# Optimization experiments

Measured on AMD Instinct MI355X. Metric: run time of the kernel, lower is better.

The kernel has to match this reference:

```python
import jax, jax.numpy as jnp
import numpy as np

B, H, LK, D = 8, 16, 4096, 128


def setup_inputs() -> dict:
    key = jax.random.key(0)
    ks = jax.random.split(key, 9)
    s = 1.0 / np.sqrt(D)
    return {
        "Q": jax.random.normal(ks[0], (B, H, 1, D), dtype=jnp.float32),
        "K": jax.random.normal(ks[1], (B, H, LK, D), dtype=jnp.float32),
        "V": jax.random.normal(ks[2], (B, H, LK, D), dtype=jnp.float32),
        "mask": jax.random.randint(ks[3], (B, H, 1, LK), 0, 2, dtype=jnp.int32),
        "scale": 1,  # accepted but unused by the original forward
        "W_pre": jax.random.normal(ks[4], (D, D), dtype=jnp.float32) * s,
        "b_pre": jax.random.normal(ks[5], (D,), dtype=jnp.float32) * s,
        "W_q": jax.random.normal(ks[6], (D, D), dtype=jnp.float32) * s,
        "W_v": jax.random.normal(ks[7], (D, 1), dtype=jnp.float32) * s,
    }


def reference(Q, K, V, mask, scale, W_pre, b_pre, W_q, W_v):
    # precompute = linear_pre(K): [B,H,LK,D]
    pre = jnp.einsum("bhkd,de->bhke", K, W_pre) + b_pre
    # targetT = linear_q(Q): [B,H,1,D], broadcast-added over keys
    tq = jnp.einsum("bhqd,de->bhqe", Q, W_q)
    tmp = jnp.tanh(pre + tq)  # [B,H,LK,D]
    # energy = linear_v(tmp) reshaped to [B,H,1,LK]
    energy = jnp.einsum("bhkd,d->bhk", tmp, W_v[:, 0])[:, :, None, :]
    m = mask.astype(energy.dtype)
    energy = energy * (1.0 - m) + m * (-1e6)
    score = jax.nn.softmax(energy, axis=-1)  # [B,H,1,LK]
    context = jnp.matmul(score, V)  # [B,H,1,D]
    return (context, score, pre)
```

## Files before the change

kernel.cpp:

```cpp
#include <hip/hip_runtime.h>
#include <hip/hip_bf16.h>
#include <math.h>

#define B_   8
#define H_   16
#define BH_  (B_*H_)
#define LK_  4096
#define D_   128

#define SEG   16
#define KSEG  (LK_/SEG)

typedef __attribute__((ext_vector_type(8))) short bf16x8;
typedef __attribute__((ext_vector_type(4))) float f32x4;

__device__ __forceinline__ float fast_tanh(float x) {
    float ax = fabsf(x);
    float e  = __expf(2.0f * ax);
    float r  = 1.0f - __fdividef(2.0f, e + 1.0f);
    return copysignf(r, x);
}

__device__ __forceinline__ void cvt_hilo(float x, unsigned short& h, unsigned short& l) {
    __hip_bfloat16 bh = __float2bfloat16(x);
    unsigned short hu = __builtin_bit_cast(unsigned short, bh);
    float hf = __uint_as_float((unsigned int)hu << 16);
    __hip_bfloat16 bl = __float2bfloat16(x - hf);
    h = hu;
    l = __builtin_bit_cast(unsigned short, bl);
}

__device__ __forceinline__ void cvt8(const float4 a, const float4 b, bf16x8& h, bf16x8& l) {
    float xs[8] = {a.x, a.y, a.z, a.w, b.x, b.y, b.z, b.w};
#pragma unroll
    for (int j = 0; j < 8; ++j) {
        unsigned short hu, lu;
        cvt_hilo(xs[j], hu, lu);
        h[j] = (short)hu;
        l[j] = (short)lu;
    }
}

__global__ void pack_kernel(const float* __restrict__ Wpre,
                            unsigned short* __restrict__ Bhi,
                            unsigned short* __restrict__ Blo) {
    int idx  = blockIdx.x * 256 + threadIdx.x;
    int j    = idx & 7;
    int lane = (idx >> 3) & 63;
    int nt   = (idx >> 9) & 7;
    int ks   = idx >> 12;
    int k    = ks * 32 + (lane >> 4) * 8 + j;
    int n    = nt * 16 + (lane & 15);
    unsigned short h, l;
    cvt_hilo(Wpre[k * D_ + n], h, l);
    Bhi[idx] = h;
    Blo[idx] = l;
}

__global__ void tq_kernel(const float* __restrict__ Q,
                          const float* __restrict__ Wq,
                          float* __restrict__ tq) {
    int bh = blockIdx.x;
    int e  = threadIdx.x;
    const float* q = Q + bh * D_;
    float acc = 0.0f;
#pragma unroll 8
    for (int d = 0; d < D_; ++d)
        acc = fmaf(q[d], Wq[d * D_ + e], acc);
    tq[bh * D_ + e] = acc;
}

__global__ void __launch_bounds__(256, 2)
main_kernel(const float* __restrict__ K,
            const unsigned short* __restrict__ Whi,
            const unsigned short* __restrict__ Wlo,
            const float* __restrict__ bpre,
            const float* __restrict__ Wv,
            const float* __restrict__ tqg,
            float* __restrict__ pre_out,
            float* __restrict__ energy_out) {
    const int t    = threadIdx.x;
    const int lane = t & 63;
    const int wv_  = t >> 6;
    const int kg   = wv_ & 1;
    const int eh   = wv_ >> 1;
    const int l15  = lane & 15;
    const int lg   = lane >> 4;
    const int bh   = blockIdx.y;
    const int kblk = blockIdx.x * 256;

    __shared__ float eLDS[2][2][64];

    bf16x8 wfh[4][4], wfl[4][4];
#pragma unroll
    for (int ks = 0; ks < 4; ++ks)
#pragma unroll
        for (int et = 0; et < 4; ++et) {
            size_t idx = (((size_t)ks * 8 + eh * 4 + et) * 64 + lane) * 8;
            wfh[ks][et] = *(const bf16x8*)(Whi + idx);
            wfl[ks][et] = *(const bf16x8*)(Wlo + idx);
        }

    float4 bpv[4], tqv[4], wvv[4];
#pragma unroll
    for (int et = 0; et < 4; ++et) {
        const int e0 = eh * 64 + et * 16 + lg * 4;
        bpv[et] = *(const float4*)(bpre + e0);
        tqv[et] = *(const float4*)(tqg + bh * D_ + e0);
        wvv[et] = *(const float4*)(Wv + e0);
    }

    const float* Kw = K + ((size_t)bh * LK_ + kblk + kg * 32 + l15) * D_ + lg * 8;

    float4 rw[2][2][2];
#pragma unroll
    for (int kt = 0; kt < 2; ++kt) {
        rw[0][kt][0] = *(const float4*)(Kw + (size_t)kt * 16 * D_);
        rw[0][kt][1] = *(const float4*)(Kw + (size_t)kt * 16 * D_ + 4);
    }

#pragma unroll
    for (int it = 0; it < 4; ++it) {
        f32x4 acc[2][4];
#pragma unroll
        for (int kt = 0; kt < 2; ++kt)
#pragma unroll
            for (int et = 0; et < 4; ++et)
                acc[kt][et] = (f32x4){0.f, 0.f, 0.f, 0.f};

#pragma unroll
        for (int ks = 0; ks < 4; ++ks) {
            const int cur = ks & 1, nxt = cur ^ 1;
            if (ks < 3) {
#pragma unroll
                for (int kt = 0; kt < 2; ++kt) {
                    const float* p = Kw + ((size_t)it * 64 + kt * 16) * D_ + (ks + 1) * 32;
                    rw[nxt][kt][0] = *(const float4*)p;
                    rw[nxt][kt][1] = *(const float4*)(p + 4);
                }
            } else if (it < 3) {
#pragma unroll
                for (int kt = 0; kt < 2; ++kt) {
                    const float* p = Kw + ((size_t)(it + 1) * 64 + kt * 16) * D_;
                    rw[nxt][kt][0] = *(const float4*)p;
                    rw[nxt][kt][1] = *(const float4*)(p + 4);
                }
            }
            bf16x8 kh[2], kl[2];
            cvt8(rw[cur][0][0], rw[cur][0][1], kh[0], kl[0]);
            cvt8(rw[cur][1][0], rw[cur][1][1], kh[1], kl[1]);
#pragma unroll
            for (int kt = 0; kt < 2; ++kt)
#pragma unroll
                for (int et = 0; et < 4; ++et) {
                    acc[kt][et] = __builtin_amdgcn_mfma_f32_16x16x32_bf16(wfh[ks][et], kh[kt], acc[kt][et], 0, 0, 0);
                    acc[kt][et] = __builtin_amdgcn_mfma_f32_16x16x32_bf16(wfl[ks][et], kh[kt], acc[kt][et], 0, 0, 0);
                    acc[kt][et] = __builtin_amdgcn_mfma_f32_16x16x32_bf16(wfh[ks][et], kl[kt], acc[kt][et], 0, 0, 0);
                }
        }

        const int kb = kblk + it * 64 + kg * 32;
#pragma unroll
        for (int kt = 0; kt < 2; ++kt) {
            float* pb = pre_out + ((size_t)bh * LK_ + kb + kt * 16 + l15) * D_ + eh * 64 + lg * 4;
            float ep = 0.0f;
#pragma unroll
            for (int et = 0; et < 4; ++et) {
                f32x4 a = acc[kt][et];
                f32x4 v;
                v[0] = a[0] + bpv[et].x;
                v[1] = a[1] + bpv[et].y;
                v[2] = a[2] + bpv[et].z;
                v[3] = a[3] + bpv[et].w;
                __builtin_nontemporal_store(v, (f32x4*)(pb + et * 16));
                ep = fmaf(fast_tanh(v[0] + tqv[et].x), wvv[et].x, ep);
                ep = fmaf(fast_tanh(v[1] + tqv[et].y), wvv[et].y, ep);
                ep = fmaf(fast_tanh(v[2] + tqv[et].z), wvv[et].z, ep);
                ep = fmaf(fast_tanh(v[3] + tqv[et].w), wvv[et].w, ep);
            }
            ep += __shfl_xor(ep, 16, 64);
            ep += __shfl_xor(ep, 32, 64);
            if (lg == 0)
                eLDS[it & 1][eh][kg * 32 + kt * 16 + l15] = ep;
        }
        asm volatile("s_waitcnt lgkmcnt(0)\n\ts_barrier" ::: "memory");
        if (t < 64) {
            float e = eLDS[it & 1][0][t] + eLDS[it & 1][1][t];
            energy_out[(size_t)bh * LK_ + kblk + it * 64 + t] = e;
        }
    }
}

__global__ void ml_kernel(const float* __restrict__ energy,
                          const int* __restrict__ mask,
                          float* __restrict__ ml) {
    const int bh = blockIdx.x;
    const int t  = threadIdx.x;
    const float* e = energy + (size_t)bh * LK_;
    const int*   m = mask   + (size_t)bh * LK_;

    float mx = -1e30f;
    for (int k = t; k < LK_; k += 256) {
        float v = m[k] ? -1.0e6f : e[k];
        mx = fmaxf(mx, v);
    }
#pragma unroll
    for (int off = 32; off > 0; off >>= 1)
        mx = fmaxf(mx, __shfl_xor(mx, off, 64));
    __shared__ float wmax[4];
    if ((t & 63) == 0) wmax[t >> 6] = mx;
    __syncthreads();
    mx = fmaxf(fmaxf(wmax[0], wmax[1]), fmaxf(wmax[2], wmax[3]));

    float sum = 0.0f;
    for (int k = t; k < LK_; k += 256) {
        float v = m[k] ? -1.0e6f : e[k];
        sum += __expf(v - mx);
    }
#pragma unroll
    for (int off = 32; off > 0; off >>= 1)
        sum += __shfl_xor(sum, off, 64);
    __shared__ float wsum[4];
    if ((t & 63) == 0) wsum[t >> 6] = sum;
    __syncthreads();
    if (t == 0) {
        ml[bh * 2]     = mx;
        ml[bh * 2 + 1] = wsum[0] + wsum[1] + wsum[2] + wsum[3];
    }
}

__global__ void score_ctx_kernel(const float* __restrict__ energy,
                                 const int* __restrict__ mask,
                                 const float* __restrict__ V,
                                 const float* __restrict__ ml,
                                 float* __restrict__ score_out,
                                 float* __restrict__ part) {
    const int seg = blockIdx.x;
    const int bh  = blockIdx.y;
    const int t   = threadIdx.x;
    const int k0  = seg * KSEG;

    __shared__ float sc[KSEG];
    __shared__ float pl[8][136];

    const float mx  = ml[bh * 2];
    const float inv = 1.0f / ml[bh * 2 + 1];

    {
        const size_t gi = (size_t)bh * LK_ + k0 + t;
        float v = mask[gi] ? -1.0e6f : energy[gi];
        float s = __expf(v - mx) * inv;
        sc[t] = s;
        score_out[gi] = s;
    }
    __syncthreads();

    const int d4 = t & 31;
    const int g  = t >> 5;
    const float* Vb = V + ((size_t)bh * LK_ + k0) * D_ + d4 * 4;
    float4 a = make_float4(0.f, 0.f, 0.f, 0.f);
#pragma unroll 4
    for (int kk = g; kk < KSEG; kk += 8) {
        float4 vv = *(const float4*)(Vb + (size_t)kk * D_);
        float s = sc[kk];
        a.x = fmaf(s, vv.x, a.x);
        a.y = fmaf(s, vv.y, a.y);
        a.z = fmaf(s, vv.z, a.z);
        a.w = fmaf(s, vv.w, a.w);
    }
    *(float4*)&pl[g][d4 * 4] = a;
    __syncthreads();

    if (t < 128) {
        float s = 0.0f;
#pragma unroll
        for (int gg = 0; gg < 8; ++gg)
            s += pl[gg][t];
        part[((size_t)bh * SEG + seg) * D_ + t] = s;
    }
}

__global__ void combine_kernel(const float* __restrict__ part,
                               float* __restrict__ ctx) {
    const int bh = blockIdx.x;
    const int d  = threadIdx.x;
    float s = 0.0f;
#pragma unroll
    for (int g = 0; g < SEG; ++g)
        s += part[((size_t)bh * SEG + g) * D_ + d];
    ctx[bh * D_ + d] = s;
}

extern "C" void kernel_launch(void* const* d_in, const int* in_sizes, int n_in,
                              void* d_out, int out_size, void* d_ws, size_t ws_size,
                              hipStream_t stream) {
    const float* Q    = (const float*)d_in[0];
    const float* K    = (const float*)d_in[1];
    const float* V    = (const float*)d_in[2];
    const int*   mask = (const int*)  d_in[3];
    const float* Wpre = (const float*)d_in[5];
    const float* bpre = (const float*)d_in[6];
    const float* Wq   = (const float*)d_in[7];
    const float* Wv   = (const float*)d_in[8];

    float* out   = (float*)d_out;
    float* ctx   = out;
    float* score = out + (size_t)BH_ * D_;
    float* pre   = score + (size_t)BH_ * LK_;

    float* w    = (float*)d_ws;
    float* tq   = w;
    float* ml   = tq + (size_t)BH_ * D_;
    float* part = ml + 2 * BH_;
    unsigned short* Whi = (unsigned short*)(part + (size_t)BH_ * SEG * D_);
    unsigned short* Wlo = Whi + 16384;

    hipLaunchKernelGGL(pack_kernel, dim3(64), dim3(256), 0, stream, Wpre, Whi, Wlo);
    hipLaunchKernelGGL(tq_kernel, dim3(BH_), dim3(D_), 0, stream, Q, Wq, tq);
    hipLaunchKernelGGL(main_kernel, dim3(LK_ / 256, BH_), dim3(256), 0, stream,
                       K, Whi, Wlo, bpre, Wv, tq, pre, score);
    hipLaunchKernelGGL(ml_kernel, dim3(BH_), dim3(256), 0, stream, score, mask, ml);
    hipLaunchKernelGGL(score_ctx_kernel, dim3(SEG, BH_), dim3(256), 0, stream,
                       score, mask, V, ml, score, part);
    hipLaunchKernelGGL(combine_kernel, dim3(BH_), dim3(D_), 0, stream, part, ctx);
}
```

Baseline: 242.1 us.

## Drop per-iteration barrier, use packed bf16 conversion and three-deep K prefetch

The main kernel no longer combines the two half-energy partials through shared memory behind a barrier on every iteration. Each wave half now writes its partial to a separate global buffer, and the following kernels add the two halves when they read them. The hi/lo bf16 split of K now uses the packed v_cvt_pk_bf16_f32 instruction instead of scalar conversions. The K register prefetch grows from double to triple buffering. In exchange the downstream kernels do extra global reads, and the main kernel holds more registers, which may strain occupancy at launch bounds 256,2.

```diff
diff --git a/kernel.cpp b/kernel.cpp
--- a/kernel.cpp
+++ b/kernel.cpp
@@ -13,12 +13,19 @@
 
 typedef __attribute__((ext_vector_type(8))) short bf16x8;
 typedef __attribute__((ext_vector_type(4))) float f32x4;
+typedef __attribute__((ext_vector_type(4))) unsigned int u32x4;
 
 __device__ __forceinline__ float fast_tanh(float x) {
     float ax = fabsf(x);
     float e  = __expf(2.0f * ax);
     float r  = 1.0f - __fdividef(2.0f, e + 1.0f);
     return copysignf(r, x);
+}
+
+__device__ __forceinline__ unsigned int cvtpk(float lo, float hi) {
+    unsigned int r;
+    asm("v_cvt_pk_bf16_f32 %0, %1, %2" : "=v"(r) : "v"(lo), "v"(hi));
+    return r;
 }
 
 __device__ __forceinline__ void cvt_hilo(float x, unsigned short& h, unsigned short& l) {
@@ -31,14 +38,22 @@
 }
 
 __device__ __forceinline__ void cvt8(const float4 a, const float4 b, bf16x8& h, bf16x8& l) {
-    float xs[8] = {a.x, a.y, a.z, a.w, b.x, b.y, b.z, b.w};
-#pragma unroll
-    for (int j = 0; j < 8; ++j) {
-        unsigned short hu, lu;
-        cvt_hilo(xs[j], hu, lu);
-        h[j] = (short)hu;
-        l[j] = (short)lu;
-    }
+    unsigned int h0 = cvtpk(a.x, a.y);
+    unsigned int h1 = cvtpk(a.z, a.w);
+    unsigned int h2 = cvtpk(b.x, b.y);
+    unsigned int h3 = cvtpk(b.z, b.w);
+    float l0 = a.x - __uint_as_float(h0 << 16);
+    float l1 = a.y - __uint_as_float(h0 & 0xFFFF0000u);
+    float l2 = a.z - __uint_as_float(h1 << 16);
+    float l3 = a.w - __uint_as_float(h1 & 0xFFFF0000u);
+    float l4 = b.x - __uint_as_float(h2 << 16);
+    float l5 = b.y - __uint_as_float(h2 & 0xFFFF0000u);
+    float l6 = b.z - __uint_as_float(h3 << 16);
+    float l7 = b.w - __uint_as_float(h3 & 0xFFFF0000u);
+    u32x4 hv = {h0, h1, h2, h3};
+    u32x4 lv = {cvtpk(l0, l1), cvtpk(l2, l3), cvtpk(l4, l5), cvtpk(l6, l7)};
+    h = __builtin_bit_cast(bf16x8, hv);
+    l = __builtin_bit_cast(bf16x8, lv);
 }
 
 __global__ void pack_kernel(const float* __restrict__ Wpre,
@@ -78,7 +93,8 @@
             const float* __restrict__ Wv,
             const float* __restrict__ tqg,
             float* __restrict__ pre_out,
-            float* __restrict__ energy_out) {
+            float* __restrict__ ep0,
+            float* __restrict__ ep1) {
     const int t    = threadIdx.x;
     const int lane = t & 63;
     const int wv_  = t >> 6;
@@ -89,8 +105,6 @@
     const int bh   = blockIdx.y;
     const int kblk = blockIdx.x * 256;
 
-    __shared__ float eLDS[2][2][64];
-
     bf16x8 wfh[4][4], wfl[4][4];
 #pragma unroll
     for (int ks = 0; ks < 4; ++ks)
@@ -112,11 +126,18 @@
 
     const float* Kw = K + ((size_t)bh * LK_ + kblk + kg * 32 + l15) * D_ + lg * 8;
 
-    float4 rw[2][2][2];
-#pragma unroll
-    for (int kt = 0; kt < 2; ++kt) {
-        rw[0][kt][0] = *(const float4*)(Kw + (size_t)kt * 16 * D_);
-        rw[0][kt][1] = *(const float4*)(Kw + (size_t)kt * 16 * D_ + 4);
+    float* epo = (eh == 0) ? ep0 : ep1;
+
+    float4 rw[3][2][2];
+#pragma unroll
+    for (int s = 0; s < 2; ++s) {
+        const int it0 = 0, ks0 = s;
+#pragma unroll
+        for (int kt = 0; kt < 2; ++kt) {
+            const float* p = Kw + ((size_t)it0 * 64 + kt * 16) * D_ + ks0 * 32;
+            rw[s][kt][0] = *(const float4*)p;
+            rw[s][kt][1] = *(const float4*)(p + 4);
+        }
     }
 
 #pragma unroll
@@ -130,25 +151,21 @@
 
 #pragma unroll
         for (int ks = 0; ks < 4; ++ks) {
-            const int cur = ks & 1, nxt = cur ^ 1;
-            if (ks < 3) {
+            const int s = it * 4 + ks;
+            if (s + 2 < 16) {
+                const int s2  = s + 2;
+                const int it2 = s2 >> 2, ks2 = s2 & 3, b2 = s2 % 3;
 #pragma unroll
                 for (int kt = 0; kt < 2; ++kt) {
-                    const float* p = Kw + ((size_t)it * 64 + kt * 16) * D_ + (ks + 1) * 32;
-                    rw[nxt][kt][0] = *(const float4*)p;
-                    rw[nxt][kt][1] = *(const float4*)(p + 4);
-                }
-            } else if (it < 3) {
-#pragma unroll
-                for (int kt = 0; kt < 2; ++kt) {
-                    const float* p = Kw + ((size_t)(it + 1) * 64 + kt * 16) * D_;
-                    rw[nxt][kt][0] = *(const float4*)p;
-                    rw[nxt][kt][1] = *(const float4*)(p + 4);
+                    const float* p = Kw + ((size_t)it2 * 64 + kt * 16) * D_ + ks2 * 32;
+                    rw[b2][kt][0] = *(const float4*)p;
+                    rw[b2][kt][1] = *(const float4*)(p + 4);
                 }
             }
+            const int cb = s % 3;
             bf16x8 kh[2], kl[2];
-            cvt8(rw[cur][0][0], rw[cur][0][1], kh[0], kl[0]);
-            cvt8(rw[cur][1][0], rw[cur][1][1], kh[1], kl[1]);
+            cvt8(rw[cb][0][0], rw[cb][0][1], kh[0], kl[0]);
+            cvt8(rw[cb][1][0], rw[cb][1][1], kh[1], kl[1]);
 #pragma unroll
             for (int kt = 0; kt < 2; ++kt)
 #pragma unroll
@@ -181,27 +198,24 @@
             ep += __shfl_xor(ep, 16, 64);
             ep += __shfl_xor(ep, 32, 64);
             if (lg == 0)
-                eLDS[it & 1][eh][kg * 32 + kt * 16 + l15] = ep;
+                epo[(size_t)bh * LK_ + kb + kt * 16 + l15] = ep;
         }
-        asm volatile("s_waitcnt lgkmcnt(0)\n\ts_barrier" ::: "memory");
-        if (t < 64) {
-            float e = eLDS[it & 1][0][t] + eLDS[it & 1][1][t];
-            energy_out[(size_t)bh * LK_ + kblk + it * 64 + t] = e;
-        }
-    }
-}
-
-__global__ void ml_kernel(const float* __restrict__ energy,
+    }
+}
+
+__global__ void ml_kernel(const float* __restrict__ ep0,
+                          const float* __restrict__ ep1,
                           const int* __restrict__ mask,
                           float* __restrict__ ml) {
     const int bh = blockIdx.x;
     const int t  = threadIdx.x;
-    const float* e = energy + (size_t)bh * LK_;
-    const int*   m = mask   + (size_t)bh * LK_;
+    const float* e0 = ep0 + (size_t)bh * LK_;
+    const float* e1 = ep1 + (size_t)bh * LK_;
+    const int*   m  = mask + (size_t)bh * LK_;
 
     float mx = -1e30f;
     for (int k = t; k < LK_; k += 256) {
-        float v = m[k] ? -1.0e6f : e[k];
+        float v = m[k] ? -1.0e6f : (e0[k] + e1[k]);
         mx = fmaxf(mx, v);
     }
 #pragma unroll
@@ -214,7 +228,7 @@
 
     float sum = 0.0f;
     for (int k = t; k < LK_; k += 256) {
-        float v = m[k] ? -1.0e6f : e[k];
+        float v = m[k] ? -1.0e6f : (e0[k] + e1[k]);
         sum += __expf(v - mx);
     }
 #pragma unroll
@@ -229,7 +243,7 @@
     }
 }
 
-__global__ void score_ctx_kernel(const float* __restrict__ energy,
+__global__ void score_ctx_kernel(const float* __restrict__ ep1,
                                  const int* __restrict__ mask,
                                  const float* __restrict__ V,
                                  const float* __restrict__ ml,
@@ -248,7 +262,7 @@
 
     {
         const size_t gi = (size_t)bh * LK_ + k0 + t;
-        float v = mask[gi] ? -1.0e6f : energy[gi];
+        float v = mask[gi] ? -1.0e6f : (score_out[gi] + ep1[gi]);
         float s = __expf(v - mx) * inv;
         sc[t] = s;
         score_out[gi] = s;
@@ -314,13 +328,14 @@
     float* part = ml + 2 * BH_;
     unsigned short* Whi = (unsigned short*)(part + (size_t)BH_ * SEG * D_);
     unsigned short* Wlo = Whi + 16384;
+    float* ep1  = (float*)(Wlo + 16384);
 
     hipLaunchKernelGGL(pack_kernel, dim3(64), dim3(256), 0, stream, Wpre, Whi, Wlo);
     hipLaunchKernelGGL(tq_kernel, dim3(BH_), dim3(D_), 0, stream, Q, Wq, tq);
     hipLaunchKernelGGL(main_kernel, dim3(LK_ / 256, BH_), dim3(256), 0, stream,
-                       K, Whi, Wlo, bpre, Wv, tq, pre, score);
-    hipLaunchKernelGGL(ml_kernel, dim3(BH_), dim3(256), 0, stream, score, mask, ml);
+                       K, Whi, Wlo, bpre, Wv, tq, pre, score, ep1);
+    hipLaunchKernelGGL(ml_kernel, dim3(BH_), dim3(256), 0, stream, score, ep1, mask, ml);
     hipLaunchKernelGGL(score_ctx_kernel, dim3(SEG, BH_), dim3(256), 0, stream,
-                       score, mask, V, ml, score, part);
+                       ep1, mask, V, ml, score, part);
     hipLaunchKernelGGL(combine_kernel, dim3(BH_), dim3(D_), 0, stream, part, ctx);
 }
```

New measurement: 256.8 us. 6.1% more time.
